# Kernel optimization log

Measured on AMD Instinct MI355X. Metric: run time of the kernel, lower is better.

## Reference

```python
import jax, jax.numpy as jnp
import numpy as np

B, QL, KVL = 2, 1024, 2048
D = 4096          # hidden_size
NH, NKV = 32, 8   # attention heads / kv heads
HD = D // NH      # head_dim = 128
INNER = 4 * D     # SwiGLU intermediate = 16384
EPS = 1e-5
THETA = 10000.0


def rope_cos_sin(seq_len, head_dim, theta):
    inv_freq = 1.0 / (theta ** (jnp.arange(0, head_dim, 2, dtype=jnp.float32) / head_dim))
    t = jnp.arange(seq_len, dtype=jnp.float32)
    freqs = jnp.outer(t, inv_freq)                      # [S, HD/2]
    emb = jnp.concatenate([freqs, freqs], axis=-1)      # [S, HD]
    return jnp.cos(emb), jnp.sin(emb)


def rotate_half(x):
    half = x.shape[-1] // 2
    return jnp.concatenate([-x[..., half:], x[..., :half]], axis=-1)


def apply_rope(x, cos, sin):
    # x: [B, H, S, HD]; cos/sin: [S, HD] broadcast over batch & heads
    return x * cos[None, None] + rotate_half(x) * sin[None, None]


def layernorm(x, w, b):
    mu = jnp.mean(x, axis=-1, keepdims=True)
    var = jnp.var(x, axis=-1, keepdims=True)
    return (x - mu) * jax.lax.rsqrt(var + EPS) * w + b


def setup_inputs() -> dict:
    key = jax.random.key(0)
    ks = jax.random.split(key, 12)
    s = 0.02
    return {
        "hidden_states": jax.random.normal(ks[0], (B, QL, D), jnp.float32),
        "encoder_hidden_states": jax.random.normal(ks[1], (B, KVL, D), jnp.float32),
        "encoder_attention_mask": jnp.ones((B, KVL), jnp.float32),
        "ln1_w": jnp.ones((D,), jnp.float32),
        "ln1_b": jnp.zeros((D,), jnp.float32),
        "q_w": jax.random.normal(ks[2], (D, D), jnp.float32) * s,        # [out, in]
        "k_w": jax.random.normal(ks[3], (NKV * HD, D), jnp.float32) * s,
        "v_w": jax.random.normal(ks[4], (NKV * HD, D), jnp.float32) * s,
        "o_w": jax.random.normal(ks[5], (D, D), jnp.float32) * s,
        "ln2_w": jnp.ones((D,), jnp.float32),
        "ln2_b": jnp.zeros((D,), jnp.float32),
        "gate_w": jax.random.normal(ks[6], (INNER, D), jnp.float32) * s,
        "up_w": jax.random.normal(ks[7], (INNER, D), jnp.float32) * s,
        "down_w": jax.random.normal(ks[8], (D, INNER), jnp.float32) * s,
    }


def reference(hidden_states, encoder_hidden_states, encoder_attention_mask,
              ln1_w, ln1_b, q_w, k_w, v_w, o_w, ln2_w, ln2_b,
              gate_w, up_w, down_w):
    residual = hidden_states
    h = layernorm(hidden_states, ln1_w, ln1_b)

    # projections
    q = (h @ q_w.T).reshape(B, QL, NH, HD).transpose(0, 2, 1, 3)                    # [B,NH,QL,HD]
    k = (encoder_hidden_states @ k_w.T).reshape(B, KVL, NKV, HD).transpose(0, 2, 1, 3)  # [B,NKV,KVL,HD]
    v = (encoder_hidden_states @ v_w.T).reshape(B, KVL, NKV, HD).transpose(0, 2, 1, 3)

    # RoPE: q uses positions 0..QL-1, k uses positions 0..KVL-1 (position_ids=None -> cos[None])
    q_cos, q_sin = rope_cos_sin(QL, HD, THETA)
    kv_cos, kv_sin = rope_cos_sin(KVL, HD, THETA)
    q = apply_rope(q, q_cos, q_sin)
    k = apply_rope(k, kv_cos, kv_sin)

    # GQA repeat_kv: each kv head repeated num_key_value_groups times consecutively
    n_rep = NH // NKV
    k = jnp.repeat(k, n_rep, axis=1)  # [B,NH,KVL,HD]
    v = jnp.repeat(v, n_rep, axis=1)

    attn = jnp.einsum('bhqd,bhkd->bhqk', q, k) / np.sqrt(HD).astype(np.float32)
    # NOTE: original code ADDS the boolean mask (True -> +1.0) to the logits
    mask = (encoder_attention_mask != 0).astype(attn.dtype)  # [B,KVL]
    attn = attn + mask[:, None, None, :]
    attn = jax.nn.softmax(attn.astype(jnp.float32), axis=-1).astype(q.dtype)

    out = jnp.einsum('bhqk,bhkd->bhqd', attn, v)        # [B,NH,QL,HD]
    out = out.transpose(0, 2, 1, 3).reshape(B, QL, D)
    attn_out = out @ o_w.T

    h = residual + attn_out
    residual = h
    h = layernorm(h, ln2_w, ln2_b)
    ff = (jax.nn.silu(h @ gate_w.T) * (h @ up_w.T)) @ down_w.T
    return residual + ff
```

## Files before the change

### kernel.cpp

```cpp
#include <hip/hip_runtime.h>
#include <hip/hip_bf16.h>
#include <math.h>

using bf16 = __hip_bfloat16;
typedef __bf16 bfv8 __attribute__((ext_vector_type(8)));
typedef float f32x4 __attribute__((ext_vector_type(4)));

__device__ __forceinline__ f32x4 mfma16(bfv8 a, bfv8 b, f32x4 c) {
    return __builtin_amdgcn_mfma_f32_16x16x32_bf16(a, b, c, 0, 0, 0);
}

__device__ __forceinline__ void gload_lds16(const void* g, void* l) {
    __builtin_amdgcn_global_load_lds(
        (const __attribute__((address_space(1))) void*)g,
        (__attribute__((address_space(3))) void*)l, 16, 0, 0);
}

__global__ void cvt_kernel(const float* __restrict__ in, bf16* __restrict__ out, long n8) {
    long u = (long)blockIdx.x * 256 + threadIdx.x;
    if (u >= n8) return;
    const float4* p = (const float4*)in + u * 2;
    float4 a = p[0], b = p[1];
    bf16 t8[8] = { __float2bfloat16(a.x), __float2bfloat16(a.y), __float2bfloat16(a.z), __float2bfloat16(a.w),
                   __float2bfloat16(b.x), __float2bfloat16(b.y), __float2bfloat16(b.z), __float2bfloat16(b.w) };
    *(int4*)(out + u * 8) = *(const int4*)t8;
}

__global__ void layernorm_kernel(const float* __restrict__ x, const float* __restrict__ gw,
                                 const float* __restrict__ gb, bf16* __restrict__ out)
{
    const int D = 4096;
    int row = blockIdx.x, t = threadIdx.x;
    const float4* xr = (const float4*)(x + (size_t)row * D);
    float4 v[4];
    float s1 = 0.f, s2 = 0.f;
#pragma unroll
    for (int j = 0; j < 4; ++j) {
        v[j] = xr[t + j * 256];
        s1 += v[j].x + v[j].y + v[j].z + v[j].w;
        s2 += v[j].x * v[j].x + v[j].y * v[j].y + v[j].z * v[j].z + v[j].w * v[j].w;
    }
#pragma unroll
    for (int d = 1; d < 64; d <<= 1) { s1 += __shfl_xor(s1, d); s2 += __shfl_xor(s2, d); }
    __shared__ float red[8];
    int wave = t >> 6, lane = t & 63;
    if (lane == 0) { red[wave] = s1; red[4 + wave] = s2; }
    __syncthreads();
    s1 = red[0] + red[1] + red[2] + red[3];
    s2 = red[4] + red[5] + red[6] + red[7];
    float mu = s1 * (1.f / 4096.f);
    float var = s2 * (1.f / 4096.f) - mu * mu;
    float rs = rsqrtf(var + 1e-5f);
    bf16* orow = out + (size_t)row * D;
#pragma unroll
    for (int j = 0; j < 4; ++j) {
        int base = (t + j * 256) * 4;
        float xs[4] = { v[j].x, v[j].y, v[j].z, v[j].w };
        bf16 o4[4];
#pragma unroll
        for (int c = 0; c < 4; ++c)
            o4[c] = __float2bfloat16((xs[c] - mu) * rs * gw[base + c] + gb[base + c]);
        *(int2*)(orow + base) = *(const int2*)o4;
    }
}

__global__ void rope_kernel(bf16* __restrict__ x, int nheads, int seqlen, long total) {
    long idx = (long)blockIdx.x * 256 + threadIdx.x;
    if (idx >= total) return;
    int j = (int)(idx & 63);
    long t2 = idx >> 6;
    int h = (int)(t2 % nheads);
    long row = t2 / nheads;
    int pos = (int)(row % seqlen);
    float inv = exp2f(-(float)j * 0.20762050593046015f);
    float ang = (float)pos * inv;
    float s, c;
    sincosf(ang, &s, &c);
    bf16* p = x + row * ((long)nheads * 128) + (long)h * 128 + j;
    float x0 = __bfloat162float(p[0]);
    float x1 = __bfloat162float(p[64]);
    p[0]  = __float2bfloat16(x0 * c - x1 * s);
    p[64] = __float2bfloat16(x1 * c + x0 * s);
}

template<int BM, int BN, int MODE, bool DUAL, int CM, int CN, int XN>
__global__ __launch_bounds__(512, 2) void gemm_p(
        const bf16* __restrict__ A, const bf16* __restrict__ W, const bf16* __restrict__ W2,
        void* __restrict__ Cout, void* __restrict__ Cout2, const void* __restrict__ aux,
        int M, int N, int K, int Nsplit)
{
    constexpr int MF = BM / 32;
    constexpr int NF = BN / 64;
    constexpr int ALD = BM / 128;
    constexpr int BLD = BN / 128;
    constexpr int SLD = ALD + BLD;
    __shared__ bf16 lds[3][(BM + BN) * 32];

    const int t = threadIdx.x;
    const int wid = t >> 6, lane = t & 63;
    const int lr = lane & 15, lg = lane >> 4;
    const int wr = wid >> 2, wc = wid & 3;
    const int bid = blockIdx.x;
    const int xcd = bid & 7, slot = bid >> 3;
    const int sm = slot / CN, sn = slot % CN;
    const int xm = xcd / XN, xn = xcd % XN;
    const int bm = (xm * CM + sm) * BM;
    const int bn = (xn * CN + sn) * BN;

    auto stage = [&](int tt, int buf) {
        const int k0 = tt * 32;
        char* ldsA = (char*)&lds[buf][0];
#pragma unroll
        for (int c = 0; c < ALD; ++c) {
            int Wb = (t + c * 512) * 16;
            int L = Wb ^ (((Wb >> 7) & 7) << 4);
            int row = L >> 6, colb = L & 63;
            gload_lds16(A + (size_t)(bm + row) * K + k0 + (colb >> 1), ldsA + Wb);
        }
        char* ldsB = (char*)&lds[buf][BM * 32];
#pragma unroll
        for (int c = 0; c < BLD; ++c) {
            int Wb = (t + c * 512) * 16;
            int L = Wb ^ (((Wb >> 7) & 7) << 4);
            int row = L >> 6, colb = L & 63;
            const bf16* src;
            if constexpr (DUAL) {
                int nr = bn + row;
                src = (nr >= Nsplit) ? W2 + (size_t)(nr - Nsplit) * K + k0 + (colb >> 1)
                                     : W  + (size_t)nr * K + k0 + (colb >> 1);
            } else {
                src = W + (size_t)(bn + row) * K + k0 + (colb >> 1);
            }
            gload_lds16(src, ldsB + Wb);
        }
    };

    const f32x4 zero4 = { 0.f, 0.f, 0.f, 0.f };
    f32x4 acc[MF][NF];
#pragma unroll
    for (int m = 0; m < MF; ++m)
#pragma unroll
        for (int n = 0; n < NF; ++n) acc[m][n] = zero4;

    const int T = K >> 5;
    stage(0, 0);
    stage(1, 1);
    if constexpr (SLD == 4) asm volatile("s_waitcnt vmcnt(4)" ::: "memory");
    else                    asm volatile("s_waitcnt vmcnt(3)" ::: "memory");
    __builtin_amdgcn_s_barrier();
    __builtin_amdgcn_sched_barrier(0);

    for (int tt = 0; tt < T; ++tt) {
        const int buf = tt % 3;
        bfv8 af[MF], bfr[NF];
#pragma unroll
        for (int m = 0; m < MF; ++m) {
            int row = wr * (BM / 2) + m * 16 + lr;
            int U = row * 64 + lg * 16;
            af[m] = *(const bfv8*)((const char*)&lds[buf][0] + (U ^ (((U >> 7) & 7) << 4)));
        }
#pragma unroll
        for (int n = 0; n < NF; ++n) {
            int row = wc * (BN / 4) + n * 16 + lr;
            int U = row * 64 + lg * 16;
            bfr[n] = *(const bfv8*)((const char*)&lds[buf][BM * 32] + (U ^ (((U >> 7) & 7) << 4)));
        }
        if (tt + 2 < T) stage(tt + 2, (tt + 2) % 3);
        __builtin_amdgcn_s_setprio(1);
#pragma unroll
        for (int m = 0; m < MF; ++m)
#pragma unroll
            for (int n = 0; n < NF; ++n)
                acc[m][n] = mfma16(af[m], bfr[n], acc[m][n]);
        __builtin_amdgcn_s_setprio(0);
        if (tt + 2 < T) {
            if constexpr (SLD == 4) asm volatile("s_waitcnt vmcnt(4)" ::: "memory");
            else                    asm volatile("s_waitcnt vmcnt(3)" ::: "memory");
        } else {
            asm volatile("s_waitcnt vmcnt(0)" ::: "memory");
        }
        __builtin_amdgcn_s_barrier();
        __builtin_amdgcn_sched_barrier(0);
    }

    const int r0 = bm + wr * (BM / 2), c0 = bn + wc * (BN / 4);
#pragma unroll
    for (int m = 0; m < MF; ++m)
#pragma unroll
        for (int n = 0; n < NF; ++n)
#pragma unroll
            for (int i = 0; i < 4; ++i) {
                int r = r0 + m * 16 + lg * 4 + i;
                int c = c0 + n * 16 + lr;
                float a = acc[m][n][i];
                if constexpr (DUAL) {
                    if (c < Nsplit) ((bf16*)Cout)[(size_t)r * Nsplit + c] = __float2bfloat16(a);
                    else ((bf16*)Cout2)[(size_t)r * (N - Nsplit) + (c - Nsplit)] = __float2bfloat16(a);
                } else {
                    size_t idx = (size_t)r * N + c;
                    if constexpr (MODE == 0) {
                        ((bf16*)Cout)[idx] = __float2bfloat16(a);
                    } else if constexpr (MODE == 1) {
                        a = a / (1.f + expf(-a));
                        ((bf16*)Cout)[idx] = __float2bfloat16(a);
                    } else if constexpr (MODE == 2) {
                        a *= __bfloat162float(((const bf16*)aux)[idx]);
                        ((bf16*)Cout)[idx] = __float2bfloat16(a);
                    } else {
                        ((float*)Cout)[idx] = a + ((const float*)aux)[idx];
                    }
                }
            }
}

template<int BN, int MODE, bool DUAL, int CM, int CN, int XN>
__global__ __launch_bounds__(512, 1) void gemm8(
        const bf16* __restrict__ A, const bf16* __restrict__ W, const bf16* __restrict__ W2,
        void* __restrict__ Cout, void* __restrict__ Cout2, const void* __restrict__ aux,
        int M, int N, int K, int Nsplit)
{
    constexpr bool BIG = (BN == 256);
    constexpr int NBUF = BIG ? 2 : 3;
    constexpr int ABY = 32768;
    constexpr int BBY = BN * 128;
    constexpr int TBY = ABY + BBY;
    __shared__ alignas(16) char lds8[NBUF * TBY];

    const int t = threadIdx.x;
    const int wid = t >> 6, lane = t & 63;
    const int lr = lane & 15, lg = lane >> 4;
    const int wrB = wid >> 2, wcB = wid & 3;
    const int wr4 = wid >> 1, wc4 = wid & 1;
    const int bid = blockIdx.x;
    const int xcd = bid & 7, slot = bid >> 3;
    const int sm = slot / CN, sn = slot % CN;
    const int xm = xcd / XN, xn = xcd % XN;
    const int bm = (xm * CM + sm) * 256;
    const int bn = (xn * CN + sn) * BN;

    auto stA = [&](int kt, int h, int buf) {
#pragma unroll
        for (int c = 0; c < 2; ++c) {
            int Wb = (t + c * 512) * 16;
            int L = Wb ^ (((Wb >> 7) & 7) << 4);
            gload_lds16(A + (size_t)(bm + h * 128 + (L >> 7)) * K + kt * 64 + ((L & 127) >> 1),
                        lds8 + buf * TBY + h * 16384 + Wb);
        }
    };
    auto stB = [&](int kt, int h, int buf) {
#pragma unroll
        for (int c = 0; c < 2; ++c) {
            int Wb = (t + c * 512) * 16;
            int L = Wb ^ (((Wb >> 7) & 7) << 4);
            int nr = bn + h * 128 + (L >> 7);
            const bf16* src;
            if constexpr (DUAL) {
                src = (nr >= Nsplit) ? W2 + (size_t)(nr - Nsplit) * K + kt * 64 + ((L & 127) >> 1)
                                     : W  + (size_t)nr * K + kt * 64 + ((L & 127) >> 1);
            } else {
                src = W + (size_t)nr * K + kt * 64 + ((L & 127) >> 1);
            }
            gload_lds16(src, lds8 + buf * TBY + ABY + h * 16384 + Wb);
        }
    };

    const f32x4 zero4 = { 0.f, 0.f, 0.f, 0.f };
    f32x4 acc[BIG ? 8 : 4][4];
#pragma unroll
    for (int m = 0; m < (BIG ? 8 : 4); ++m)
#pragma unroll
        for (int n = 0; n < 4; ++n) acc[m][n] = zero4;

    bfv8 af[4][2], bfr[2][2][2];
    bfv8 afs[2][2], bfs[4][2];

#define LOADA(BUF, MH) do {                                                   \
    const char* _ba = lds8 + (BUF) * TBY;                                     \
    _Pragma("unroll") for (int m = 0; m < 4; ++m)                             \
    _Pragma("unroll") for (int ks = 0; ks < 2; ++ks) {                        \
        int row = wrB * 128 + (MH) * 64 + m * 16 + lr;                        \
        int U = row * 128 + ks * 64 + lg * 16;                                \
        af[m][ks] = *(const bfv8*)(_ba + (U ^ ((row & 7) << 4)));             \
    } } while (0)

#define LOADB(BUF, NH) do {                                                   \
    const char* _bb = lds8 + (BUF) * TBY + ABY;                               \
    _Pragma("unroll") for (int n = 0; n < 2; ++n)                             \
    _Pragma("unroll") for (int ks = 0; ks < 2; ++ks) {                        \
        int row = wcB * 64 + (NH) * 32 + n * 16 + lr;                         \
        int U = row * 128 + ks * 64 + lg * 16;                                \
        bfr[NH][n][ks] = *(const bfv8*)(_bb + (U ^ ((row & 7) << 4)));        \
    } } while (0)

#define MFMAQ(MH, NH) do {                                                    \
    _Pragma("unroll") for (int m = 0; m < 4; ++m)                             \
    _Pragma("unroll") for (int n = 0; n < 2; ++n) {                           \
        acc[(MH)*4+m][(NH)*2+n] = mfma16(af[m][0], bfr[NH][n][0], acc[(MH)*4+m][(NH)*2+n]); \
        acc[(MH)*4+m][(NH)*2+n] = mfma16(af[m][1], bfr[NH][n][1], acc[(MH)*4+m][(NH)*2+n]); \
    } } while (0)

#define LOADA_S(BUF, MH) do {                                                 \
    const char* _ba = lds8 + (BUF) * TBY;                                     \
    _Pragma("unroll") for (int m = 0; m < 2; ++m)                             \
    _Pragma("unroll") for (int ks = 0; ks < 2; ++ks) {                        \
        int row = wr4 * 64 + (MH) * 32 + m * 16 + lr;                         \
        int U = row * 128 + ks * 64 + lg * 16;                                \
        afs[m][ks] = *(const bfv8*)(_ba + (U ^ ((row & 7) << 4)));            \
    } } while (0)

#define LOADB_S(BUF) do {                                                     \
    const char* _bb = lds8 + (BUF) * TBY + ABY;                               \
    _Pragma("unroll") for (int n = 0; n < 4; ++n)                             \
    _Pragma("unroll") for (int ks = 0; ks < 2; ++ks) {                        \
        int row = wc4 * 64 + n * 16 + lr;                                     \
        int U = row * 128 + ks * 64 + lg * 16;                                \
        bfs[n][ks] = *(const bfv8*)(_bb + (U ^ ((row & 7) << 4)));            \
    } } while (0)

#define MFMAQ_S(MH) do {                                                      \
    _Pragma("unroll") for (int m = 0; m < 2; ++m)                             \
    _Pragma("unroll") for (int n = 0; n < 4; ++n) {                           \
        acc[(MH)*2+m][n] = mfma16(afs[m][0], bfs[n][0], acc[(MH)*2+m][n]);    \
        acc[(MH)*2+m][n] = mfma16(afs[m][1], bfs[n][1], acc[(MH)*2+m][n]);    \
    } } while (0)

#define PH_TOP() do { __builtin_amdgcn_s_barrier();                           \
    asm volatile("s_waitcnt lgkmcnt(0)" ::: "memory");                        \
    __builtin_amdgcn_sched_barrier(0);                                        \
    __builtin_amdgcn_s_setprio(1); } while (0)

#define PH_END() do { __builtin_amdgcn_s_setprio(0);                          \
    __builtin_amdgcn_s_barrier(); } while (0)

#define GATE(LIVE) do { __builtin_amdgcn_s_setprio(0);                        \
    if (LIVE) { if constexpr (BIG) asm volatile("s_waitcnt vmcnt(4)" ::: "memory"); \
                else               asm volatile("s_waitcnt vmcnt(6)" ::: "memory"); } \
    else      asm volatile("s_waitcnt vmcnt(0)" ::: "memory");                \
    __builtin_amdgcn_s_barrier(); } while (0)

    const int T = K >> 6;
    const int T2 = T >> 1;

    if constexpr (BIG) {
        stA(0, 0, 0); stA(0, 1, 0); stB(0, 0, 0); stB(0, 1, 0);
        stB(1, 0, 1); stB(1, 1, 1);
        asm volatile("s_waitcnt vmcnt(4)" ::: "memory");
        __builtin_amdgcn_s_barrier();

        for (int tt = 0; tt < T2; ++tt) {
            const int o = 2 * tt + 1, e2 = 2 * tt + 2, o2 = 2 * tt + 3;
            const bool le = (e2 < T), lo = (o2 < T);
            LOADA(0, 0); LOADB(0, 0); stA(o, 0, 1);
            PH_TOP(); MFMAQ(0, 0); PH_END();
            LOADB(0, 1); stA(o, 1, 1);
            PH_TOP(); MFMAQ(0, 1); PH_END();
            LOADA(0, 1); if (le) stB(e2, 0, 0);
            PH_TOP(); MFMAQ(1, 1); PH_END();
            if (le) stB(e2, 1, 0);
            PH_TOP(); MFMAQ(1, 0); GATE(le);
            LOADA(1, 0); LOADB(1, 0); if (le) stA(e2, 0, 0);
            PH_TOP(); MFMAQ(0, 0); PH_END();
            LOADB(1, 1); if (le) stA(e2, 1, 0);
            PH_TOP(); MFMAQ(0, 1); PH_END();
            LOADA(1, 1); if (lo) stB(o2, 0, 1);
            PH_TOP(); MFMAQ(1, 1); PH_END();
            if (lo) stB(o2, 1, 1);
            PH_TOP(); MFMAQ(1, 0); GATE(le);
        }
    } else {
        stA(0, 0, 0); stB(0, 0, 0); stA(0, 1, 0);
        stA(1, 0, 1); stB(1, 0, 1); stA(1, 1, 1);
        asm volatile("s_waitcnt vmcnt(6)" ::: "memory");
        __builtin_amdgcn_s_barrier();

        int bE = 0, bO = 1, bN = 2;
        for (int tt = 0; tt < T2; ++tt) {
            const int e2 = 2 * tt + 2, o2 = 2 * tt + 3;
            const bool le = (e2 < T), lo = (o2 < T);
            LOADA_S(bE, 0); LOADB_S(bE); if (le) { stA(e2, 0, bN); stB(e2, 0, bN); }
            PH_TOP(); MFMAQ_S(0); PH_END();
            LOADA_S(bE, 1); if (le) stA(e2, 1, bN);
            PH_TOP(); MFMAQ_S(1); GATE(le);
            LOADA_S(bO, 0); LOADB_S(bO); if (lo) { stA(o2, 0, bE); stB(o2, 0, bE); }
            PH_TOP(); MFMAQ_S(0); PH_END();
            LOADA_S(bO, 1); if (lo) stA(o2, 1, bE);
            PH_TOP(); MFMAQ_S(1); GATE(lo);
            int nE = bN, nO = bE, nN = bO;
            bE = nE; bO = nO; bN = nN;
        }
    }

#undef LOADA
#undef LOADB
#undef MFMAQ
#undef LOADA_S
#undef LOADB_S
#undef MFMAQ_S
#undef PH_TOP
#undef PH_END
#undef GATE

    const int r0 = bm + (BIG ? wrB * 128 : wr4 * 64);
    const int c0 = bn + (BIG ? wcB * 64 : wc4 * 64);
#pragma unroll
    for (int mg = 0; mg < (BIG ? 8 : 4); ++mg)
#pragma unroll
        for (int ng = 0; ng < 4; ++ng)
#pragma unroll
            for (int i = 0; i < 4; ++i) {
                int r = r0 + mg * 16 + lg * 4 + i;
                int c = c0 + ng * 16 + lr;
                float a = acc[mg][ng][i];
                if constexpr (DUAL) {
                    if (c < Nsplit) ((bf16*)Cout)[(size_t)r * Nsplit + c] = __float2bfloat16(a);
                    else ((bf16*)Cout2)[(size_t)r * (N - Nsplit) + (c - Nsplit)] = __float2bfloat16(a);
                } else {
                    size_t idx = (size_t)r * N + c;
                    if constexpr (MODE == 0) {
                        ((bf16*)Cout)[idx] = __float2bfloat16(a);
                    } else if constexpr (MODE == 1) {
                        a = a / (1.f + expf(-a));
                        ((bf16*)Cout)[idx] = __float2bfloat16(a);
                    } else if constexpr (MODE == 2) {
                        a *= __bfloat162float(((const bf16*)aux)[idx]);
                        ((bf16*)Cout)[idx] = __float2bfloat16(a);
                    } else {
                        ((float*)Cout)[idx] = a + ((const float*)aux)[idx];
                    }
                }
            }
}

__global__ void transpose_v(const bf16* __restrict__ vb, bf16* __restrict__ vt) {
    __shared__ bf16 tile[64][68];
    int kv0 = blockIdx.x * 64, c0 = blockIdx.y * 64, b = blockIdx.z;
    int t = threadIdx.x;
    int cr = t & 15, rr = t >> 4;
#pragma unroll
    for (int j = 0; j < 4; ++j) {
        int r = rr + j * 16;
        *(int2*)&tile[r][cr * 4] = *(const int2*)&vb[(size_t)(b * 2048 + kv0 + r) * 1024 + c0 + cr * 4];
    }
    __syncthreads();
#pragma unroll
    for (int j = 0; j < 4; ++j) {
        int cc = rr + j * 16;
        bf16 tmp[4];
#pragma unroll
        for (int q = 0; q < 4; ++q) tmp[q] = tile[cr * 4 + q][cc];
        *(int2*)&vt[(size_t)(b * 1024 + c0 + cc) * 2048 + kv0 + cr * 4] = *(const int2*)tmp;
    }
}

__global__ __launch_bounds__(256) void attn_kernel(
    const bf16* __restrict__ Q, const bf16* __restrict__ Kb, const bf16* __restrict__ Vt,
    const float* __restrict__ mask, bf16* __restrict__ O)
{
    const int QL_ = 1024, KVL_ = 2048;
    const float scale = 0.08838834764831845f;
    int qt = blockIdx.x, h = blockIdx.y, b = blockIdx.z;
    int t = threadIdx.x, wave = t >> 6, lane = t & 63;
    int lr = lane & 15, lg = lane >> 4;
    int g = h >> 2;
    __shared__ bf16 Ksm[2][64 * 128];
    __shared__ bf16 Vsm[2][128 * 64];
    __shared__ bf16 Psm[4][16 * 72];
    int q0 = qt * 64 + wave * 16;

    auto stage = [&](int buf, int kv0) {
#pragma unroll
        for (int p2 = 0; p2 < 4; ++p2) {
            int Wb = (p2 * 256 + t) * 16;
            int row = Wb >> 8;
            int col = ((Wb & 255) ^ ((row & 7) << 4)) >> 1;
            gload_lds16(Kb + (size_t)(b * KVL_ + kv0 + row) * 1024 + g * 128 + col,
                        (char*)&Ksm[buf][0] + Wb);
        }
#pragma unroll
        for (int p2 = 0; p2 < 4; ++p2) {
            int Wb = (p2 * 256 + t) * 16;
            int row = Wb >> 7;
            int col = ((Wb & 127) ^ ((row & 7) << 4)) >> 1;
            gload_lds16(Vt + (size_t)(b * 1024 + g * 128 + row) * 2048 + kv0 + col,
                        (char*)&Vsm[buf][0] + Wb);
        }
    };

    const bf16* qptr = Q + (size_t)(b * QL_ + q0 + lr) * 4096 + h * 128;
    bfv8 qf[4];
#pragma unroll
    for (int kc = 0; kc < 4; ++kc) qf[kc] = *(const bfv8*)(qptr + kc * 32 + lg * 8);

    const f32x4 zero4 = { 0.f, 0.f, 0.f, 0.f };
    f32x4 accO[8];
#pragma unroll
    for (int dt = 0; dt < 8; ++dt) accO[dt] = zero4;
    float mrow[4] = { -1e30f, -1e30f, -1e30f, -1e30f };
    float lrow[4] = { 0.f, 0.f, 0.f, 0.f };

    stage(0, 0);
    int buf = 0;
    const int NT = KVL_ / 64;
    for (int tt = 0; tt < NT; ++tt) {
        const int kv0 = tt * 64;
        if (tt + 1 < NT) {
            stage(buf ^ 1, kv0 + 64);
            asm volatile("s_waitcnt vmcnt(8)" ::: "memory");
        } else {
            asm volatile("s_waitcnt vmcnt(0)" ::: "memory");
        }
        __builtin_amdgcn_s_barrier();

        f32x4 s[4];
#pragma unroll
        for (int ct = 0; ct < 4; ++ct) {
            s[ct] = zero4;
#pragma unroll
            for (int kc = 0; kc < 4; ++kc) {
                int row = ct * 16 + lr;
                int U = row * 256 + kc * 64 + lg * 16;
                bfv8 kf = *(const bfv8*)((const char*)&Ksm[buf][0] + (U ^ ((row & 7) << 4)));
                s[ct] = mfma16(qf[kc], kf, s[ct]);
            }
            float mv = mask[(size_t)b * KVL_ + kv0 + ct * 16 + lr];
            mv = (mv != 0.f) ? 1.f : 0.f;
#pragma unroll
            for (int i = 0; i < 4; ++i) s[ct][i] = s[ct][i] * scale + mv;
        }

        float rmx[4], mnew[4], corr[4], psum[4];
#pragma unroll
        for (int i = 0; i < 4; ++i) {
            rmx[i] = fmaxf(fmaxf(s[0][i], s[1][i]), fmaxf(s[2][i], s[3][i]));
#pragma unroll
            for (int d = 1; d < 16; d <<= 1) rmx[i] = fmaxf(rmx[i], __shfl_xor(rmx[i], d));
            mnew[i] = fmaxf(mrow[i], rmx[i]);
            corr[i] = expf(mrow[i] - mnew[i]);
            psum[i] = 0.f;
        }
#pragma unroll
        for (int ct = 0; ct < 4; ++ct)
#pragma unroll
            for (int i = 0; i < 4; ++i) {
                float pv = expf(s[ct][i] - mnew[i]);
                psum[i] += pv;
                Psm[wave][(lg * 4 + i) * 72 + ct * 16 + lr] = __float2bfloat16(pv);
            }
#pragma unroll
        for (int i = 0; i < 4; ++i) {
#pragma unroll
            for (int d = 1; d < 16; d <<= 1) psum[i] += __shfl_xor(psum[i], d);
            lrow[i] = lrow[i] * corr[i] + psum[i];
            mrow[i] = mnew[i];
        }
#pragma unroll
        for (int dt = 0; dt < 8; ++dt)
#pragma unroll
            for (int i = 0; i < 4; ++i) accO[dt][i] *= corr[i];

        bfv8 pf0 = *(const bfv8*)&Psm[wave][lr * 72 + 0 * 32 + lg * 8];
        bfv8 pf1 = *(const bfv8*)&Psm[wave][lr * 72 + 1 * 32 + lg * 8];
#pragma unroll
        for (int dt = 0; dt < 8; ++dt) {
            int row = dt * 16 + lr;
            int U0 = row * 128 + 0 * 64 + lg * 16;
            int U1 = row * 128 + 1 * 64 + lg * 16;
            bfv8 vf0 = *(const bfv8*)((const char*)&Vsm[buf][0] + (U0 ^ ((row & 7) << 4)));
            bfv8 vf1 = *(const bfv8*)((const char*)&Vsm[buf][0] + (U1 ^ ((row & 7) << 4)));
            accO[dt] = mfma16(pf0, vf0, accO[dt]);
            accO[dt] = mfma16(pf1, vf1, accO[dt]);
        }
        __builtin_amdgcn_s_barrier();
        buf ^= 1;
    }

    float invl[4];
#pragma unroll
    for (int i = 0; i < 4; ++i) invl[i] = 1.f / lrow[i];
#pragma unroll
    for (int dt = 0; dt < 8; ++dt)
#pragma unroll
        for (int i = 0; i < 4; ++i)
            O[(size_t)(b * QL_ + q0 + lg * 4 + i) * 4096 + h * 128 + dt * 16 + lr] =
                __float2bfloat16(accO[dt][i] * invl[i]);
}

extern "C" void kernel_launch(void* const* d_in, const int* in_sizes, int n_in,
                              void* d_out, int out_size, void* d_ws, size_t ws_size,
                              hipStream_t stream) {
    const float* hidden = (const float*)d_in[0];
    const float* enc    = (const float*)d_in[1];
    const float* mask   = (const float*)d_in[2];
    const float* ln1w   = (const float*)d_in[3];
    const float* ln1b   = (const float*)d_in[4];
    const float* qw     = (const float*)d_in[5];
    const float* kw     = (const float*)d_in[6];
    const float* vw     = (const float*)d_in[7];
    const float* ow     = (const float*)d_in[8];
    const float* ln2w   = (const float*)d_in[9];
    const float* ln2b   = (const float*)d_in[10];
    const float* gatew  = (const float*)d_in[11];
    const float* upw    = (const float*)d_in[12];
    const float* downw  = (const float*)d_in[13];
    float* out = (float*)d_out;

    char* ws = (char*)d_ws;
    bf16*  wbuf  = (bf16*)(ws);
    bf16*  wbuf2 = (bf16*)(ws + 8388608);
    bf16*  h1    = (bf16*)(ws + 134217728);
    bf16*  encb  = (bf16*)(ws + 150994944);
    bf16*  qb    = (bf16*)(ws + 184549376);
    bf16*  kb    = (bf16*)(ws + 201326592);
    bf16*  vb    = (bf16*)(ws + 209715200);
    bf16*  attno = (bf16*)(ws + 218103808);
    float* h2    = (float*)(ws + 234881024);
    bf16*  vt    = (bf16*)(ws + 234881024);
    bf16*  h2n   = (bf16*)(ws + 268435456);
    bf16*  g1    = (bf16*)(ws + 285212672);

    auto cvt = [&](const float* src, bf16* dst, long n) {
        cvt_kernel<<<(int)(n / 2048), 256, 0, stream>>>(src, dst, n / 8);
    };

    cvt(enc, encb, 16777216L);
    layernorm_kernel<<<2048, 256, 0, stream>>>(hidden, ln1w, ln1b, h1);

    cvt(qw, wbuf, 16777216L);
    gemm_p<128, 256, 0, false, 8, 4, 4><<<256, 512, 0, stream>>>(
        h1, wbuf, nullptr, qb, nullptr, nullptr, 2048, 4096, 4096, 0);
    rope_kernel<<<16384, 256, 0, stream>>>(qb, 32, 1024, 2048L * 32 * 64);

    cvt(kw, wbuf, 4194304L);
    cvt(vw, wbuf2, 4194304L);
    gemm_p<128, 256, 0, true, 8, 4, 2><<<256, 512, 0, stream>>>(
        encb, wbuf, wbuf2, kb, vb, nullptr, 4096, 2048, 4096, 1024);
    rope_kernel<<<8192, 256, 0, stream>>>(kb, 8, 2048, 4096L * 8 * 64);
    transpose_v<<<dim3(32, 16, 2), 256, 0, stream>>>(vb, vt);

    attn_kernel<<<dim3(16, 32, 2), 256, 0, stream>>>(qb, kb, vt, mask, attno);

    cvt(ow, wbuf, 16777216L);
    gemm_p<128, 256, 3, false, 8, 4, 4><<<256, 512, 0, stream>>>(
        attno, wbuf, nullptr, h2, nullptr, hidden, 2048, 4096, 4096, 0);

    layernorm_kernel<<<2048, 256, 0, stream>>>(h2, ln2w, ln2b, h2n);

    cvt(gatew, wbuf, 67108864L);
    gemm8<256, 1, false, 8, 8, 8><<<512, 512, 0, stream>>>(
        h2n, wbuf, nullptr, g1, nullptr, nullptr, 2048, 16384, 4096, 0);
    cvt(upw, wbuf, 67108864L);
    gemm8<256, 2, false, 8, 8, 8><<<512, 512, 0, stream>>>(
        h2n, wbuf, nullptr, g1, nullptr, g1, 2048, 16384, 4096, 0);

    cvt(downw, wbuf, 67108864L);
    gemm8<128, 3, false, 8, 4, 8><<<256, 512, 0, stream>>>(
        g1, wbuf, nullptr, out, nullptr, h2, 2048, 4096, 16384, 0);
}
```

Baseline: 1.496 ms.

## Fuse next-GEMM weight fp32-to-bf16 conversion into preceding GEMM main loops

```diff
diff --git a/kernel.cpp b/kernel.cpp
--- a/kernel.cpp
+++ b/kernel.cpp
@@ -83,11 +83,12 @@
     p[64] = __float2bfloat16(x1 * c + x0 * s);
 }
 
-template<int BM, int BN, int MODE, bool DUAL, int CM, int CN, int XN>
+template<int BM, int BN, int MODE, bool DUAL, int CM, int CN, int XN, int SIDE>
 __global__ __launch_bounds__(512, 2) void gemm_p(
         const bf16* __restrict__ A, const bf16* __restrict__ W, const bf16* __restrict__ W2,
         void* __restrict__ Cout, void* __restrict__ Cout2, const void* __restrict__ aux,
-        int M, int N, int K, int Nsplit)
+        int M, int N, int K, int Nsplit,
+        const float* __restrict__ SF, bf16* __restrict__ SD)
 {
     constexpr int MF = BM / 32;
     constexpr int NF = BN / 64;
@@ -151,6 +152,11 @@
     __builtin_amdgcn_sched_barrier(0);
 
     for (int tt = 0; tt < T; ++tt) {
+        float4 sv;
+        if constexpr (SIDE == 1) {
+            size_t si = (((size_t)bid * (size_t)T + tt) * 512 + t) * 4;
+            sv = *(const float4*)(SF + si);
+        }
         const int buf = tt % 3;
         bfv8 af[MF], bfr[NF];
 #pragma unroll
@@ -181,6 +187,12 @@
         }
         __builtin_amdgcn_s_barrier();
         __builtin_amdgcn_sched_barrier(0);
+        if constexpr (SIDE == 1) {
+            size_t si = (((size_t)bid * (size_t)T + tt) * 512 + t) * 4;
+            bf16 o4[4] = { __float2bfloat16(sv.x), __float2bfloat16(sv.y),
+                           __float2bfloat16(sv.z), __float2bfloat16(sv.w) };
+            *(int2*)(SD + si) = *(const int2*)o4;
+        }
     }
 
     const int r0 = bm + wr * (BM / 2), c0 = bn + wc * (BN / 4);
@@ -213,11 +225,12 @@
             }
 }
 
-template<int BN, int MODE, bool DUAL, int CM, int CN, int XN>
+template<int BN, int MODE, bool DUAL, int CM, int CN, int XN, int SIDE>
 __global__ __launch_bounds__(512, 1) void gemm8(
         const bf16* __restrict__ A, const bf16* __restrict__ W, const bf16* __restrict__ W2,
         void* __restrict__ Cout, void* __restrict__ Cout2, const void* __restrict__ aux,
-        int M, int N, int K, int Nsplit)
+        int M, int N, int K, int Nsplit,
+        const float* __restrict__ SF, bf16* __restrict__ SD)
 {
     constexpr bool BIG = (BN == 256);
     constexpr int NBUF = BIG ? 2 : 3;
@@ -348,6 +361,12 @@
         __builtin_amdgcn_s_barrier();
 
         for (int tt = 0; tt < T2; ++tt) {
+            float4 sva, svb;
+            if constexpr (SIDE == 2) {
+                size_t si = (((size_t)bid * (size_t)T2 + tt) * 512 + t) * 8;
+                sva = *(const float4*)(SF + si);
+                svb = *(const float4*)(SF + si + 4);
+            }
             const int o = 2 * tt + 1, e2 = 2 * tt + 2, o2 = 2 * tt + 3;
             const bool le = (e2 < T), lo = (o2 < T);
             LOADA(0, 0); LOADB(0, 0); stA(o, 0, 1);
@@ -366,6 +385,14 @@
             PH_TOP(); MFMAQ(1, 1); PH_END();
             if (lo) stB(o2, 1, 1);
             PH_TOP(); MFMAQ(1, 0); GATE(le);
+            if constexpr (SIDE == 2) {
+                size_t si = (((size_t)bid * (size_t)T2 + tt) * 512 + t) * 8;
+                bf16 o8[8] = { __float2bfloat16(sva.x), __float2bfloat16(sva.y),
+                               __float2bfloat16(sva.z), __float2bfloat16(sva.w),
+                               __float2bfloat16(svb.x), __float2bfloat16(svb.y),
+                               __float2bfloat16(svb.z), __float2bfloat16(svb.w) };
+                *(int4*)(SD + si) = *(const int4*)o8;
+            }
         }
     } else {
         stA(0, 0, 0); stB(0, 0, 0); stA(0, 1, 0);
@@ -603,56 +630,105 @@
     const float* upw    = (const float*)d_in[12];
     const float* downw  = (const float*)d_in[13];
     float* out = (float*)d_out;
-
     char* ws = (char*)d_ws;
-    bf16*  wbuf  = (bf16*)(ws);
-    bf16*  wbuf2 = (bf16*)(ws + 8388608);
-    bf16*  h1    = (bf16*)(ws + 134217728);
-    bf16*  encb  = (bf16*)(ws + 150994944);
-    bf16*  qb    = (bf16*)(ws + 184549376);
-    bf16*  kb    = (bf16*)(ws + 201326592);
-    bf16*  vb    = (bf16*)(ws + 209715200);
-    bf16*  attno = (bf16*)(ws + 218103808);
-    float* h2    = (float*)(ws + 234881024);
-    bf16*  vt    = (bf16*)(ws + 234881024);
-    bf16*  h2n   = (bf16*)(ws + 268435456);
-    bf16*  g1    = (bf16*)(ws + 285212672);
 
     auto cvt = [&](const float* src, bf16* dst, long n) {
         cvt_kernel<<<(int)(n / 2048), 256, 0, stream>>>(src, dst, n / 8);
     };
 
-    cvt(enc, encb, 16777216L);
-    layernorm_kernel<<<2048, 256, 0, stream>>>(hidden, ln1w, ln1b, h1);
-
-    cvt(qw, wbuf, 16777216L);
-    gemm_p<128, 256, 0, false, 8, 4, 4><<<256, 512, 0, stream>>>(
-        h1, wbuf, nullptr, qb, nullptr, nullptr, 2048, 4096, 4096, 0);
-    rope_kernel<<<16384, 256, 0, stream>>>(qb, 32, 1024, 2048L * 32 * 64);
-
-    cvt(kw, wbuf, 4194304L);
-    cvt(vw, wbuf2, 4194304L);
-    gemm_p<128, 256, 0, true, 8, 4, 2><<<256, 512, 0, stream>>>(
-        encb, wbuf, wbuf2, kb, vb, nullptr, 4096, 2048, 4096, 1024);
-    rope_kernel<<<8192, 256, 0, stream>>>(kb, 8, 2048, 4096L * 8 * 64);
-    transpose_v<<<dim3(32, 16, 2), 256, 0, stream>>>(vb, vt);
-
-    attn_kernel<<<dim3(16, 32, 2), 256, 0, stream>>>(qb, kb, vt, mask, attno);
-
-    cvt(ow, wbuf, 16777216L);
-    gemm_p<128, 256, 3, false, 8, 4, 4><<<256, 512, 0, stream>>>(
-        attno, wbuf, nullptr, h2, nullptr, hidden, 2048, 4096, 4096, 0);
-
-    layernorm_kernel<<<2048, 256, 0, stream>>>(h2, ln2w, ln2b, h2n);
-
-    cvt(gatew, wbuf, 67108864L);
-    gemm8<256, 1, false, 8, 8, 8><<<512, 512, 0, stream>>>(
-        h2n, wbuf, nullptr, g1, nullptr, nullptr, 2048, 16384, 4096, 0);
-    cvt(upw, wbuf, 67108864L);
-    gemm8<256, 2, false, 8, 8, 8><<<512, 512, 0, stream>>>(
-        h2n, wbuf, nullptr, g1, nullptr, g1, 2048, 16384, 4096, 0);
-
-    cvt(downw, wbuf, 67108864L);
-    gemm8<128, 3, false, 8, 4, 8><<<256, 512, 0, stream>>>(
-        g1, wbuf, nullptr, out, nullptr, h2, 2048, 4096, 16384, 0);
-}
+    if (ws_size >= 385875968ULL) {
+        bf16* WA   = (bf16*)(ws);
+        bf16* h1   = (bf16*)(ws);
+        bf16* qwB  = (bf16*)(ws + 16777216);
+        bf16* kwB  = (bf16*)(ws + 50331648);
+        bf16* vwB  = (bf16*)(ws + 58720256);
+        bf16* WB   = (bf16*)(ws + 134217728);
+        bf16* encb = (bf16*)(ws + 134217728);
+        bf16* qb   = (bf16*)(ws + 167772160);
+        bf16* kb   = (bf16*)(ws + 184549376);
+        bf16* vb   = (bf16*)(ws + 192937984);
+        bf16* vt   = (bf16*)(ws + 201326592);
+        bf16* attno= (bf16*)(ws + 209715200);
+        bf16* owB  = (bf16*)(ws + 226492416);
+        float* h2  = (float*)(ws + 268435456);
+        bf16* h2n  = (bf16*)(ws + 301989888);
+        bf16* g1   = (bf16*)(ws + 318767104);
+
+        cvt(enc, encb, 16777216L);
+        layernorm_kernel<<<2048, 256, 0, stream>>>(hidden, ln1w, ln1b, h1);
+
+        cvt(qw, qwB, 16777216L);
+        gemm_p<128, 256, 0, false, 8, 4, 4, 0><<<256, 512, 0, stream>>>(
+            h1, qwB, nullptr, qb, nullptr, nullptr, 2048, 4096, 4096, 0, nullptr, nullptr);
+        rope_kernel<<<16384, 256, 0, stream>>>(qb, 32, 1024, 2048L * 32 * 64);
+
+        cvt(kw, kwB, 4194304L);
+        cvt(vw, vwB, 4194304L);
+        gemm_p<128, 256, 0, true, 8, 4, 2, 0><<<256, 512, 0, stream>>>(
+            encb, kwB, vwB, kb, vb, nullptr, 4096, 2048, 4096, 1024, nullptr, nullptr);
+        rope_kernel<<<8192, 256, 0, stream>>>(kb, 8, 2048, 4096L * 8 * 64);
+        transpose_v<<<dim3(32, 16, 2), 256, 0, stream>>>(vb, vt);
+
+        attn_kernel<<<dim3(16, 32, 2), 256, 0, stream>>>(qb, kb, vt, mask, attno);
+
+        cvt(ow, owB, 16777216L);
+        gemm_p<128, 256, 3, false, 8, 4, 4, 1><<<256, 512, 0, stream>>>(
+            attno, owB, nullptr, h2, nullptr, hidden, 2048, 4096, 4096, 0, gatew, WA);
+
+        layernorm_kernel<<<2048, 256, 0, stream>>>(h2, ln2w, ln2b, h2n);
+
+        gemm8<256, 1, false, 8, 8, 8, 2><<<512, 512, 0, stream>>>(
+            h2n, WA, nullptr, g1, nullptr, nullptr, 2048, 16384, 4096, 0, upw, WB);
+        gemm8<256, 2, false, 8, 8, 8, 2><<<512, 512, 0, stream>>>(
+            h2n, WB, nullptr, g1, nullptr, g1, 2048, 16384, 4096, 0, downw, WA);
+        gemm8<128, 3, false, 8, 4, 8, 0><<<256, 512, 0, stream>>>(
+            g1, WA, nullptr, out, nullptr, h2, 2048, 4096, 16384, 0, nullptr, nullptr);
+    } else {
+        bf16*  wbuf  = (bf16*)(ws);
+        bf16*  wbuf2 = (bf16*)(ws + 8388608);
+        bf16*  h1    = (bf16*)(ws + 134217728);
+        bf16*  encb  = (bf16*)(ws + 150994944);
+        bf16*  qb    = (bf16*)(ws + 184549376);
+        bf16*  kb    = (bf16*)(ws + 201326592);
+        bf16*  vb    = (bf16*)(ws + 209715200);
+        bf16*  attno = (bf16*)(ws + 218103808);
+        float* h2    = (float*)(ws + 234881024);
+        bf16*  vt    = (bf16*)(ws + 234881024);
+        bf16*  h2n   = (bf16*)(ws + 268435456);
+        bf16*  g1    = (bf16*)(ws + 285212672);
+
+        cvt(enc, encb, 16777216L);
+        layernorm_kernel<<<2048, 256, 0, stream>>>(hidden, ln1w, ln1b, h1);
+
+        cvt(qw, wbuf, 16777216L);
+        gemm_p<128, 256, 0, false, 8, 4, 4, 0><<<256, 512, 0, stream>>>(
+            h1, wbuf, nullptr, qb, nullptr, nullptr, 2048, 4096, 4096, 0, nullptr, nullptr);
+        rope_kernel<<<16384, 256, 0, stream>>>(qb, 32, 1024, 2048L * 32 * 64);
+
+        cvt(kw, wbuf, 4194304L);
+        cvt(vw, wbuf2, 4194304L);
+        gemm_p<128, 256, 0, true, 8, 4, 2, 0><<<256, 512, 0, stream>>>(
+            encb, wbuf, wbuf2, kb, vb, nullptr, 4096, 2048, 4096, 1024, nullptr, nullptr);
+        rope_kernel<<<8192, 256, 0, stream>>>(kb, 8, 2048, 4096L * 8 * 64);
+        transpose_v<<<dim3(32, 16, 2), 256, 0, stream>>>(vb, vt);
+
+        attn_kernel<<<dim3(16, 32, 2), 256, 0, stream>>>(qb, kb, vt, mask, attno);
+
+        cvt(ow, wbuf, 16777216L);
+        gemm_p<128, 256, 3, false, 8, 4, 4, 0><<<256, 512, 0, stream>>>(
+            attno, wbuf, nullptr, h2, nullptr, hidden, 2048, 4096, 4096, 0, nullptr, nullptr);
+
+        layernorm_kernel<<<2048, 256, 0, stream>>>(h2, ln2w, ln2b, h2n);
+
+        cvt(gatew, wbuf, 67108864L);
+        gemm8<256, 1, false, 8, 8, 8, 0><<<512, 512, 0, stream>>>(
+            h2n, wbuf, nullptr, g1, nullptr, nullptr, 2048, 16384, 4096, 0, nullptr, nullptr);
+        cvt(upw, wbuf, 67108864L);
+        gemm8<256, 2, false, 8, 8, 8, 0><<<512, 512, 0, stream>>>(
+            h2n, wbuf, nullptr, g1, nullptr, g1, 2048, 16384, 4096, 0, nullptr, nullptr);
+
+        cvt(downw, wbuf, 67108864L);
+        gemm8<128, 3, false, 8, 4, 8, 0><<<256, 512, 0, stream>>>(
+            g1, wbuf, nullptr, out, nullptr, h2, 2048, 4096, 16384, 0, nullptr, nullptr);
+    }
+}
```

After: 2.030 ms. +35.7%, slower.
